# Performance work log

Measured on AMD Instinct MI355X. Metric: run time of the kernel, lower is better.

## Reference

```python
import jax, jax.numpy as jnp
import numpy as np

BATCH, NVIS, NHID, NCOND = 4096, 1024, 4096, 512


def setup_inputs() -> dict:
    key = jax.random.key(0)
    ks = jax.random.split(key, 6)
    return {
        "visible_data": jax.random.uniform(ks[0], (BATCH, NVIS), dtype=jnp.float32),
        "cond_data": jax.random.normal(ks[1], (BATCH, NCOND), dtype=jnp.float32),
        # uniform noise replaces torch.bernoulli's internal RNG: sample = (noise < p)
        "noise": jax.random.uniform(ks[2], (BATCH, NHID), dtype=jnp.float32),
        "W": jax.random.normal(ks[3], (NVIS, NHID), dtype=jnp.float32) * 0.1,
        "b": jnp.zeros((1, NVIS), dtype=jnp.float32),
        "c": jnp.zeros((1, NHID), dtype=jnp.float32),
        "A": jax.random.normal(ks[4], (NCOND, NVIS), dtype=jnp.float32) * 0.1,
        "B": jax.random.normal(ks[5], (NCOND, NHID), dtype=jnp.float32) * 0.1,
    }


def reference(visible_data, cond_data, noise, W, b, c, A, B):
    # sample_h_given_vu: sigmoid(v@W + u@B + c), bernoulli sample via uniform noise
    h1_mean = jax.nn.sigmoid(visible_data @ W + cond_data @ B + c)  # [B, nhid]
    h1_sample = (noise < h1_mean).astype(h1_mean.dtype)
    # sample_v_given_hu (binary): L1-normalized exp == softmax, then argmax one-hot
    pre = h1_sample @ W.T + cond_data @ A + b  # [B, nvis]
    v1_mean = jax.nn.softmax(pre, axis=1)
    max_idx = jnp.argmax(v1_mean, axis=1)
    v1_sample = jax.nn.one_hot(max_idx, pre.shape[1], dtype=pre.dtype)
    return v1_sample
```

## Files before the change

kernel.cpp:

```cpp
#include <hip/hip_runtime.h>
#include <math.h>

static constexpr int BATCH = 4096;
static constexpr int NVIS  = 1024;
static constexpr int NHID  = 4096;
static constexpr int NCOND = 512;

typedef __attribute__((ext_vector_type(8))) short bf16x8;
typedef __attribute__((ext_vector_type(4))) float f32x4;
typedef __attribute__((ext_vector_type(4))) int   i32x4;

static constexpr unsigned HCAP = 131072;
static constexpr unsigned RCAP = 256;
static constexpr size_t MB = 1u << 20;

static constexpr size_t F_WT0   = 0;
static constexpr size_t F_WT1   = F_WT0  + 8*MB;
static constexpr size_t F_BMT0  = F_WT1  + 8*MB;
static constexpr size_t F_BMT1  = F_BMT0 + 4*MB;
static constexpr size_t F_AT0   = F_BMT1 + 4*MB;
static constexpr size_t F_AT1   = F_AT0  + 1*MB;
static constexpr size_t F_V0    = F_AT1  + 1*MB;
static constexpr size_t F_V1    = F_V0   + 8*MB;
static constexpr size_t F_U0    = F_V1   + 8*MB;
static constexpr size_t F_U1    = F_U0   + 4*MB;
static constexpr size_t F_QH    = F_U1   + 4*MB;
static constexpr size_t F_QL    = F_QH   + 4*MB;
static constexpr size_t F_SINV  = F_QL   + 4*MB;
static constexpr size_t F_H     = F_SINV + 8*MB;
static constexpr size_t F_BB    = F_H    + 32*MB;
static constexpr size_t F_HFLAG = F_BB   + 1*MB;
static constexpr size_t F_RFLAG = F_HFLAG + 512*1024;
static constexpr size_t F_RBEST = F_RFLAG + 16384;
static constexpr size_t F_CNT   = F_RBEST + 16384;
static constexpr size_t F_PREB  = F_CNT  + 256;
static constexpr size_t WS_FULL = F_PREB + 2*MB;

__device__ __forceinline__ void gload16(const void* g, void* l) {
    __builtin_amdgcn_global_load_lds(
        (const __attribute__((address_space(1))) void*)g,
        (__attribute__((address_space(3))) void*)l, 16, 0, 0);
}

__device__ __forceinline__ void split1(float x, unsigned short& hi, unsigned short& lo) {
    unsigned u = __float_as_uint(x);
    unsigned r = u + 0x7FFFu + ((u >> 16) & 1u);
    hi = (unsigned short)(r >> 16);
    float rem = x - __uint_as_float(r & 0xFFFF0000u);
    unsigned u2 = __float_as_uint(rem);
    unsigned r2 = u2 + 0x7FFFu + ((u2 >> 16) & 1u);
    lo = (unsigned short)(r2 >> 16);
}

__device__ __forceinline__ void merge3(float& b, unsigned& ix, float& s,
                                       float b2, unsigned i2, float s2) {
    if (b2 > b || (b2 == b && i2 < ix)) { s = fmaxf(b, s2); b = b2; ix = i2; }
    else                                { s = fmaxf(s, b2); }
}

__global__ void kz_zero(unsigned* c) { if (threadIdx.x < 64) c[threadIdx.x] = 0; }

__global__ __launch_bounds__(256) void transpose_split(
    const float* __restrict__ src, int R, int C,
    unsigned short* __restrict__ d0, unsigned short* __restrict__ d1) {
    __shared__ float tile[32][33];
    const int c0 = blockIdx.x * 32, r0 = blockIdx.y * 32;
    const int tx = threadIdx.x & 31, ty = threadIdx.x >> 5;
#pragma unroll
    for (int e = 0; e < 4; ++e)
        tile[ty + e * 8][tx] = src[(size_t)(r0 + ty + e * 8) * C + c0 + tx];
    __syncthreads();
#pragma unroll
    for (int e = 0; e < 4; ++e) {
        int c = c0 + ty + e * 8;
        unsigned short hi, lo;
        split1(tile[tx][ty + e * 8], hi, lo);
        d0[(size_t)c * R + r0 + tx] = hi;
        d1[(size_t)c * R + r0 + tx] = lo;
    }
}

__global__ __launch_bounds__(256) void transpose_f32(
    const float* __restrict__ src, int R, int C, float* __restrict__ dst) {
    __shared__ float tile[32][33];
    const int c0 = blockIdx.x * 32, r0 = blockIdx.y * 32;
    const int tx = threadIdx.x & 31, ty = threadIdx.x >> 5;
#pragma unroll
    for (int e = 0; e < 4; ++e)
        tile[ty + e * 8][tx] = src[(size_t)(r0 + ty + e * 8) * C + c0 + tx];
    __syncthreads();
#pragma unroll
    for (int e = 0; e < 4; ++e)
        dst[(size_t)(c0 + ty + e * 8) * R + r0 + tx] = tile[tx][ty + e * 8];
}

__global__ __launch_bounds__(256) void split_planes(
    const float* __restrict__ src, int n4,
    unsigned short* __restrict__ p0, unsigned short* __restrict__ p1) {
    for (int i = blockIdx.x * 256 + threadIdx.x; i < n4; i += gridDim.x * 256) {
        float4 v = ((const float4*)src)[i];
        unsigned short h0,h1,h2,h3,l0,l1,l2,l3;
        split1(v.x,h0,l0); split1(v.y,h1,l1); split1(v.z,h2,l2); split1(v.w,h3,l3);
        ((ushort4*)p0)[i] = make_ushort4(h0,h1,h2,h3);
        ((ushort4*)p1)[i] = make_ushort4(l0,l1,l2,l3);
    }
}

__global__ __launch_bounds__(256) void quantize_w(
    const float* __restrict__ W, signed char* __restrict__ QH,
    signed char* __restrict__ QL, float* __restrict__ SINV) {
    __shared__ float red[256];
    const int i = blockIdx.x, t = threadIdx.x;
    const float* row = W + (size_t)i * NHID;
    float4 v[4];
    float mx = 0.f;
#pragma unroll
    for (int e = 0; e < 4; ++e) {
        v[e] = *(const float4*)(row + e * 1024 + t * 4);
        mx = fmaxf(mx, fmaxf(fmaxf(fabsf(v[e].x), fabsf(v[e].y)),
                             fmaxf(fabsf(v[e].z), fabsf(v[e].w))));
    }
    red[t] = mx; __syncthreads();
    for (int s = 128; s; s >>= 1) {
        if (t < s) red[t] = fmaxf(red[t], red[t + s]);
        __syncthreads();
    }
    const float rm = fmaxf(red[0], 1e-30f);
    const float sc = 32256.f / rm;
    if (t == 0) SINV[i] = rm / 32256.f;
#pragma unroll
    for (int e = 0; e < 4; ++e) {
        const float* pv = (const float*)&v[e];
        unsigned ph = 0, pl = 0;
#pragma unroll
        for (int j = 0; j < 4; ++j) {
            int wq = (int)lrintf(pv[j] * sc);
            int hi = (wq + 128) >> 8;
            int lo = wq - (hi << 8);
            ph |= ((unsigned)hi & 0xFFu) << (8 * j);
            pl |= ((unsigned)lo & 0xFFu) << (8 * j);
        }
        *(unsigned*)(QH + (size_t)i * NHID + e * 1024 + t * 4) = ph;
        *(unsigned*)(QL + (size_t)i * NHID + e * 1024 + t * 4) = pl;
    }
}

__global__ __launch_bounds__(512, 1) void k1_b64(
    const float* __restrict__ noise,
    const unsigned short* __restrict__ V0, const unsigned short* __restrict__ V1,
    const unsigned short* __restrict__ U0, const unsigned short* __restrict__ U1,
    const unsigned short* __restrict__ WT0, const unsigned short* __restrict__ WT1,
    const unsigned short* __restrict__ BmT0, const unsigned short* __restrict__ BmT1,
    const float* __restrict__ cvec, unsigned char* __restrict__ hout,
    unsigned* __restrict__ hcnt, unsigned* __restrict__ hflag)
{
    __shared__ __align__(16) unsigned short As0[256][64], As1[256][64],
                                            Bs0[256][64], Bs1[256][64];
    const int t = threadIdx.x, lane = t & 63, wid = t >> 6;
    const int g = lane >> 4, cc = lane & 15;
    const int wrow = wid >> 2, wcol = wid & 3;
    const int nwg = gridDim.x * gridDim.y;
    const int bid = blockIdx.y * gridDim.x + blockIdx.x;
    const int q = nwg >> 3;
    const int swz = (bid & 7) * q + (bid >> 3);
    const int b0 = (swz / gridDim.x) * 256;
    const int j0 = (swz % gridDim.x) * 256;

    f32x4 acc[8][4] = {};
    bf16x8 a0q[4], a1q[4];
    bf16x8 b0a[2][2], b1a[2][2];

    auto lba = [&](int r, int kk) {
        return (size_t)r * 128 + (size_t)(((kk << 2) | g) ^ (r & 7)) * 16;
    };
    auto readA = [&](int mh, int kk) {
#pragma unroll
        for (int k = 0; k < 4; ++k) {
            int r = wrow * 128 + (4 * mh + k) * 16 + cc;
            a0q[k] = *(const bf16x8*)((const char*)As0 + lba(r, kk));
            a1q[k] = *(const bf16x8*)((const char*)As1 + lba(r, kk));
        }
    };
    auto readB = [&](int nh, int kk) {
#pragma unroll
        for (int k = 0; k < 2; ++k) {
            int n = wcol * 64 + (2 * nh + k) * 16 + cc;
            b0a[nh][k] = *(const bf16x8*)((const char*)Bs0 + lba(n, kk));
            b1a[nh][k] = *(const bf16x8*)((const char*)Bs1 + lba(n, kk));
        }
    };
    auto mfma24 = [&](int mh, int nh) {
#pragma unroll
        for (int k = 0; k < 4; ++k)
#pragma unroll
            for (int n = 0; n < 2; ++n) {
                f32x4 c = acc[4 * mh + k][2 * nh + n];
                c = __builtin_amdgcn_mfma_f32_16x16x32_bf16(a0q[k], b0a[nh][n], c, 0, 0, 0);
                c = __builtin_amdgcn_mfma_f32_16x16x32_bf16(a0q[k], b1a[nh][n], c, 0, 0, 0);
                c = __builtin_amdgcn_mfma_f32_16x16x32_bf16(a1q[k], b0a[nh][n], c, 0, 0, 0);
                acc[4 * mh + k][2 * nh + n] = c;
            }
    };

    for (int tt = 0; tt < 24; ++tt) {
        const unsigned short *A0_, *A1_, *B0_, *B1_; int K_, k0_;
        if (tt < 16) { A0_ = V0; A1_ = V1; B0_ = WT0; B1_ = WT1; K_ = 1024; k0_ = tt * 64; }
        else         { A0_ = U0; A1_ = U1; B0_ = BmT0; B1_ = BmT1; K_ = 512; k0_ = (tt - 16) * 64; }
        __syncthreads();
#pragma unroll
        for (int e = 0; e < 4; ++e) {
            int idx = t + e * 512;
            int r = idx >> 3, p = idx & 7;
            int s = p ^ (r & 7);
            size_t ga = (size_t)(b0 + r) * K_ + k0_ + s * 8;
            size_t gb = (size_t)(j0 + r) * K_ + k0_ + s * 8;
            size_t ldd = (size_t)idx * 16;
            gload16(A0_ + ga, (char*)As0 + ldd);
            gload16(A1_ + ga, (char*)As1 + ldd);
            gload16(B0_ + gb, (char*)Bs0 + ldd);
            gload16(B1_ + gb, (char*)Bs1 + ldd);
        }
        __syncthreads();
#pragma unroll
        for (int kk = 0; kk < 2; ++kk) {
            readA(0, kk); readB(0, kk);
            __builtin_amdgcn_s_setprio(1); mfma24(0, 0); __builtin_amdgcn_s_setprio(0);
            readB(1, kk);
            __builtin_amdgcn_s_setprio(1); mfma24(0, 1); __builtin_amdgcn_s_setprio(0);
            readA(1, kk);
            __builtin_amdgcn_s_setprio(1); mfma24(1, 0); mfma24(1, 1); __builtin_amdgcn_s_setprio(0);
        }
    }

#pragma unroll
    for (int ni = 0; ni < 4; ++ni) {
        int j = j0 + wcol * 64 + ni * 16 + cc;
        float cj = cvec[j];
#pragma unroll
        for (int mi = 0; mi < 8; ++mi) {
#pragma unroll
            for (int i = 0; i < 4; ++i) {
                int b = b0 + wrow * 128 + mi * 16 + g * 4 + i;
                float z = acc[mi][ni][i] + cj;
                float m = 1.0f / (1.0f + __expf(-z));
                float nv = noise[(size_t)b * NHID + j];
                hout[(size_t)b * NHID + j] = (nv < m) ? (unsigned char)1 : (unsigned char)0;
                if (fabsf(nv - m) < 2.5e-4f) {
                    unsigned p = atomicAdd(hcnt, 1u);
                    if (p < HCAP) hflag[p] = ((unsigned)b << 12) | (unsigned)j;
                }
            }
        }
    }
}

__global__ __launch_bounds__(512, 2) void k2_i8(
    const unsigned char* __restrict__ hbf,
    const unsigned short* __restrict__ U0, const unsigned short* __restrict__ U1,
    const signed char* __restrict__ QH, const signed char* __restrict__ QL,
    const float* __restrict__ SINV,
    const unsigned short* __restrict__ AT0, const unsigned short* __restrict__ AT1,
    const float* __restrict__ bvec, float4* __restrict__ blockbest)
{
    __shared__ __align__(16) char smem[32768];
    __shared__ float4 mbuf[4][128];
    const int t = threadIdx.x, lane = t & 63, wid = t >> 6;
    const int g = lane >> 4, cc = lane & 15;
    const int wrow = wid >> 2, wcol = wid & 3;
    const int pcb = (g ^ ((cc >> 1) & 3)) * 16;
    const int nwg = gridDim.x * gridDim.y;
    const int bid = blockIdx.y * gridDim.x + blockIdx.x;
    const int q = nwg >> 3;
    const int swz = (bid & 7) * q + (bid >> 3);
    const int b0 = (swz / gridDim.x) * 128;
    const int i0 = (swz % gridDim.x) * 128;

    char* Ah  = smem;
    char* Qhs = smem + 8192;
    char* Qls = smem + 16384;

    i32x4 ah[4][2] = {}, al[4][2] = {};

    for (int k0 = 0; k0 < NHID; k0 += 64) {
        __syncthreads();
        {
            int r = t >> 2, s = t & 3, sc = s ^ ((r >> 1) & 3);
            size_t off = (size_t)r * 64 + s * 16;
            gload16(hbf + (size_t)(b0 + r) * NHID + k0 + sc * 16, Ah + off);
            gload16(QH + (size_t)(i0 + r) * NHID + k0 + sc * 16, Qhs + off);
            gload16(QL + (size_t)(i0 + r) * NHID + k0 + sc * 16, Qls + off);
        }
        __syncthreads();
        i32x4 bh[2], bl[2];
#pragma unroll
        for (int ni = 0; ni < 2; ++ni) {
            int n = wcol * 32 + ni * 16 + cc;
            bh[ni] = *(const i32x4*)(Qhs + (size_t)n * 64 + pcb);
            bl[ni] = *(const i32x4*)(Qls + (size_t)n * 64 + pcb);
        }
#pragma unroll
        for (int mi = 0; mi < 4; ++mi) {
            i32x4 a = *(const i32x4*)(Ah + (size_t)(wrow * 64 + mi * 16 + cc) * 64 + pcb);
#pragma unroll
            for (int ni = 0; ni < 2; ++ni) {
                ah[mi][ni] = __builtin_amdgcn_mfma_i32_16x16x64_i8(a, bh[ni], ah[mi][ni], 0, 0, 0);
                al[mi][ni] = __builtin_amdgcn_mfma_i32_16x16x64_i8(a, bl[ni], al[mi][ni], 0, 0, 0);
            }
        }
    }
    f32x4 acc[4][2];
#pragma unroll
    for (int ni = 0; ni < 2; ++ni) {
        int col = i0 + wcol * 32 + ni * 16 + cc;
        float sv = SINV[col];
#pragma unroll
        for (int mi = 0; mi < 4; ++mi)
#pragma unroll
            for (int e = 0; e < 4; ++e)
                acc[mi][ni][e] = fmaf(256.f, (float)ah[mi][ni][e], (float)al[mi][ni][e]) * sv;
    }

    char* As0 = smem;
    char* As1 = smem + 8192;
    char* Bs0 = smem + 16384;
    char* Bs1 = smem + 24576;
    for (int k0 = 0; k0 < NCOND; k0 += 32) {
        __syncthreads();
        {
            int r = t >> 2, s = t & 3, sc = s ^ ((r >> 1) & 3);
            size_t off = (size_t)r * 64 + s * 16;
            size_t ga = (size_t)(b0 + r) * NCOND + k0 + sc * 8;
            gload16(U0 + ga, As0 + off);
            gload16(U1 + ga, As1 + off);
            size_t go = (size_t)(i0 + r) * NCOND + k0 + sc * 8;
            gload16(AT0 + go, Bs0 + off);
            gload16(AT1 + go, Bs1 + off);
        }
        __syncthreads();
        bf16x8 bb0[2], bb1[2];
#pragma unroll
        for (int ni = 0; ni < 2; ++ni) {
            int n = wcol * 32 + ni * 16 + cc;
            bb0[ni] = *(const bf16x8*)(Bs0 + (size_t)n * 64 + pcb);
            bb1[ni] = *(const bf16x8*)(Bs1 + (size_t)n * 64 + pcb);
        }
#pragma unroll
        for (int mi = 0; mi < 4; ++mi) {
            int r = wrow * 64 + mi * 16 + cc;
            bf16x8 a0 = *(const bf16x8*)(As0 + (size_t)r * 64 + pcb);
            bf16x8 a1 = *(const bf16x8*)(As1 + (size_t)r * 64 + pcb);
#pragma unroll
            for (int ni = 0; ni < 2; ++ni) {
                acc[mi][ni] = __builtin_amdgcn_mfma_f32_16x16x32_bf16(a0, bb0[ni], acc[mi][ni], 0, 0, 0);
                acc[mi][ni] = __builtin_amdgcn_mfma_f32_16x16x32_bf16(a0, bb1[ni], acc[mi][ni], 0, 0, 0);
                acc[mi][ni] = __builtin_amdgcn_mfma_f32_16x16x32_bf16(a1, bb0[ni], acc[mi][ni], 0, 0, 0);
            }
        }
    }

#pragma unroll
    for (int ni = 0; ni < 2; ++ni) {
        int colb = i0 + wcol * 32 + ni * 16 + cc;
        float bb = bvec[colb];
#pragma unroll
        for (int mi = 0; mi < 4; ++mi)
#pragma unroll
            for (int i = 0; i < 4; ++i) acc[mi][ni][i] += bb;
    }
#pragma unroll
    for (int mi = 0; mi < 4; ++mi) {
#pragma unroll
        for (int i = 0; i < 4; ++i) {
            float best = acc[mi][0][i];
            unsigned bidx = (unsigned)(i0 + wcol * 32 + cc);
            float sec = -3.4e38f;
            merge3(best, bidx, sec, acc[mi][1][i],
                   (unsigned)(i0 + wcol * 32 + 16 + cc), -3.4e38f);
#pragma unroll
            for (int m = 1; m < 16; m <<= 1) {
                float ob = __shfl_xor(best, m);
                unsigned oi = __shfl_xor(bidx, m);
                float os = __shfl_xor(sec, m);
                merge3(best, bidx, sec, ob, oi, os);
            }
            if (cc == 0)
                mbuf[wcol][wrow * 64 + mi * 16 + g * 4 + i] =
                    make_float4(best, sec, __uint_as_float(bidx), 0.f);
        }
    }
    __syncthreads();
    if (t < 128) {
        float4 f0 = mbuf[0][t];
        float best = f0.x, sec = f0.y;
        unsigned bidx = __float_as_uint(f0.z);
#pragma unroll
        for (int wq = 1; wq < 4; ++wq) {
            float4 fq = mbuf[wq][t];
            merge3(best, bidx, sec, fq.x, __float_as_uint(fq.z), fq.y);
        }
        blockbest[(size_t)(b0 + t) * 8 + (unsigned)(i0 >> 7)] =
            make_float4(best, sec, __uint_as_float(bidx), 0.f);
    }
}

__global__ __launch_bounds__(256) void k5_recheck_h(
    const float* __restrict__ vd, const float* __restrict__ cd, const float* __restrict__ noise,
    const float* __restrict__ WTf, const float* __restrict__ BmTf, const float* __restrict__ cvec,
    const unsigned* __restrict__ hcnt, const unsigned* __restrict__ hflag,
    unsigned char* __restrict__ h) {
    const int gw = (blockIdx.x * 256 + threadIdx.x) >> 6, lane = threadIdx.x & 63;
    const int nw = gridDim.x * 4;
    unsigned n = *hcnt; if (n > HCAP) n = HCAP;
    for (unsigned e = gw; e < n; e += nw) {
        unsigned p = hflag[e];
        int b = p >> 12, j = p & 4095;
        double s = 0.0;
        for (int k = lane; k < NVIS; k += 64)
            s += (double)vd[(size_t)b * NVIS + k] * (double)WTf[(size_t)j * NVIS + k];
        for (int k = lane; k < NCOND; k += 64)
            s += (double)cd[(size_t)b * NCOND + k] * (double)BmTf[(size_t)j * NCOND + k];
        for (int m = 32; m; m >>= 1) s += __shfl_xor(s, m);
        if (lane == 0) {
            double z = s + (double)cvec[j];
            double mm = 1.0 / (1.0 + exp(-z));
            h[(size_t)b * NHID + j] =
                ((double)noise[(size_t)b * NHID + j] < mm) ? (unsigned char)1 : (unsigned char)0;
        }
    }
}

__global__ __launch_bounds__(256) void k3_merge8(
    const float4* __restrict__ blockbest, unsigned* __restrict__ rowbest,
    unsigned* __restrict__ rcnt, unsigned* __restrict__ rowflag) {
    const int t = threadIdx.x;
    const int row = blockIdx.x * 32 + (t >> 3), e = t & 7;
    float4 f = blockbest[(size_t)row * 8 + e];
    float best = f.x, sec = f.y;
    unsigned idx = __float_as_uint(f.z);
#pragma unroll
    for (int m = 1; m < 8; m <<= 1) {
        float ob = __shfl_xor(best, m);
        unsigned oi = __shfl_xor(idx, m);
        float os = __shfl_xor(sec, m);
        merge3(best, idx, sec, ob, oi, os);
    }
    if (e == 0) {
        rowbest[row] = idx;
        if (best - sec < 4e-3f) {
            unsigned p = atomicAdd(rcnt, 1u);
            if (p < 4096) rowflag[p] = (unsigned)row;
        }
    }
}

__global__ __launch_bounds__(256) void k_onehot(const unsigned* __restrict__ rowbest,
                                                float* __restrict__ out) {
    const int row = blockIdx.x;
    const unsigned idx = rowbest[row];
    const int base = threadIdx.x * 4;
    float4 o;
    o.x = (base + 0 == (int)idx) ? 1.f : 0.f;
    o.y = (base + 1 == (int)idx) ? 1.f : 0.f;
    o.z = (base + 2 == (int)idx) ? 1.f : 0.f;
    o.w = (base + 3 == (int)idx) ? 1.f : 0.f;
    *(float4*)(out + (size_t)row * NVIS + base) = o;
}

__global__ __launch_bounds__(256) void k6_rows_pre(
    const unsigned char* __restrict__ h, const float* __restrict__ cd,
    const float* __restrict__ W, const float* __restrict__ ATf, const float* __restrict__ bvec,
    const unsigned* __restrict__ rcnt, const unsigned* __restrict__ rowflag,
    double* __restrict__ prebuf) {
    const int gw = (blockIdx.x * 256 + threadIdx.x) >> 6, lane = threadIdx.x & 63;
    const int nw = gridDim.x * 4;
    unsigned n = *rcnt; if (n > RCAP) n = RCAP;
    for (unsigned e = gw; e < n * 1024u; e += nw) {
        int ri = e >> 10, i = e & 1023;
        int b = (int)rowflag[ri];
        double s = 0.0;
        for (int k = lane; k < NHID; k += 64) {
            double hv = h[(size_t)b * NHID + k] ? 1.0 : 0.0;
            s += hv * (double)W[(size_t)i * NHID + k];
        }
        for (int k = lane; k < NCOND; k += 64)
            s += (double)cd[(size_t)b * NCOND + k] * (double)ATf[(size_t)i * NCOND + k];
        for (int m = 32; m; m >>= 1) s += __shfl_xor(s, m);
        if (lane == 0) prebuf[(size_t)ri * 1024 + i] = s + (double)bvec[i];
    }
}

__global__ __launch_bounds__(256) void k6_rows_argmax(
    const unsigned* __restrict__ rcnt, const unsigned* __restrict__ rowflag,
    const double* __restrict__ prebuf, float* __restrict__ out) {
    __shared__ double sv[256];
    __shared__ int si[256];
    unsigned n = *rcnt; if (n > RCAP) n = RCAP;
    const int t = threadIdx.x;
    for (unsigned ri = blockIdx.x; ri < n; ri += gridDim.x) {
        const int row = (int)rowflag[ri];
        const double* pr = prebuf + (size_t)ri * 1024;
        double best = pr[t * 4];
        int bi = t * 4;
#pragma unroll
        for (int e = 1; e < 4; ++e) {
            double v = pr[t * 4 + e];
            if (v > best) { best = v; bi = t * 4 + e; }
        }
        sv[t] = best; si[t] = bi;
        __syncthreads();
        for (int s = 128; s; s >>= 1) {
            if (t < s) {
                double v2 = sv[t + s]; int i2 = si[t + s];
                if (v2 > sv[t] || (v2 == sv[t] && i2 < si[t])) { sv[t] = v2; si[t] = i2; }
            }
            __syncthreads();
        }
        const int amax = si[0];
        const int base = t * 4;
        float4 o;
        o.x = (base + 0 == amax) ? 1.f : 0.f;
        o.y = (base + 1 == amax) ? 1.f : 0.f;
        o.z = (base + 2 == amax) ? 1.f : 0.f;
        o.w = (base + 3 == amax) ? 1.f : 0.f;
        *(float4*)(out + (size_t)row * NVIS + base) = o;
        __syncthreads();
    }
}

extern "C" void kernel_launch(void* const* d_in, const int* in_sizes, int n_in,
                              void* d_out, int out_size, void* d_ws, size_t ws_size,
                              hipStream_t stream) {
    const float* vd = (const float*)d_in[0];
    const float* cd = (const float*)d_in[1];
    const float* nz = (const float*)d_in[2];
    const float* W  = (const float*)d_in[3];
    const float* bv = (const float*)d_in[4];
    const float* cv = (const float*)d_in[5];
    const float* Am = (const float*)d_in[6];
    const float* Bm = (const float*)d_in[7];
    float* out = (float*)d_out;
    char* w = (char*)d_ws;

    unsigned short* WT0  = (unsigned short*)(w + F_WT0);
    unsigned short* WT1  = (unsigned short*)(w + F_WT1);
    unsigned short* BmT0 = (unsigned short*)(w + F_BMT0);
    unsigned short* BmT1 = (unsigned short*)(w + F_BMT1);
    unsigned short* AT0  = (unsigned short*)(w + F_AT0);
    unsigned short* AT1  = (unsigned short*)(w + F_AT1);
    unsigned short* V0   = (unsigned short*)(w + F_V0);
    unsigned short* V1   = (unsigned short*)(w + F_V1);
    unsigned short* U0   = (unsigned short*)(w + F_U0);
    unsigned short* U1   = (unsigned short*)(w + F_U1);
    signed char*    QH   = (signed char*)(w + F_QH);
    signed char*    QL   = (signed char*)(w + F_QL);
    float*          SINV = (float*)(w + F_SINV);
    unsigned char*  hbf  = (unsigned char*)(w + F_H);
    float4*   blockbest  = (float4*)(w + F_BB);
    unsigned* hflag      = (unsigned*)(w + F_HFLAG);
    unsigned* rowflag    = (unsigned*)(w + F_RFLAG);
    unsigned* rowbest    = (unsigned*)(w + F_RBEST);
    unsigned* counters   = (unsigned*)(w + F_CNT);
    double*   prebuf     = (double*)(w + F_PREB);
    unsigned* hcnt = &counters[0];
    unsigned* rcnt = &counters[1];
    float* WTf32  = (float*)(w + F_V0);
    float* BmTf32 = (float*)(w + F_WT0);
    float* ATf32  = (float*)(w + F_WT1);

    dim3 blk(256);
    kz_zero<<<1, 64, 0, stream>>>(counters);
    transpose_split<<<dim3(NHID / 32, NVIS / 32), blk, 0, stream>>>(W, NVIS, NHID, WT0, WT1);
    transpose_split<<<dim3(NHID / 32, NCOND / 32), blk, 0, stream>>>(Bm, NCOND, NHID, BmT0, BmT1);
    transpose_split<<<dim3(NVIS / 32, NCOND / 32), blk, 0, stream>>>(Am, NCOND, NVIS, AT0, AT1);
    split_planes<<<2048, blk, 0, stream>>>(vd, BATCH * NVIS / 4, V0, V1);
    split_planes<<<2048, blk, 0, stream>>>(cd, BATCH * NCOND / 4, U0, U1);
    quantize_w<<<NVIS, blk, 0, stream>>>(W, QH, QL, SINV);
    k1_b64<<<dim3(NHID / 256, BATCH / 256), 512, 0, stream>>>(
        nz, V0, V1, U0, U1, WT0, WT1, BmT0, BmT1, cv, hbf, hcnt, hflag);
    transpose_f32<<<dim3(NHID / 32, NVIS / 32), blk, 0, stream>>>(W, NVIS, NHID, WTf32);
    transpose_f32<<<dim3(NHID / 32, NCOND / 32), blk, 0, stream>>>(Bm, NCOND, NHID, BmTf32);
    transpose_f32<<<dim3(NVIS / 32, NCOND / 32), blk, 0, stream>>>(Am, NCOND, NVIS, ATf32);
    k5_recheck_h<<<256, blk, 0, stream>>>(vd, cd, nz, WTf32, BmTf32, cv, hcnt, hflag, hbf);
    k2_i8<<<dim3(NVIS / 128, BATCH / 128), 512, 0, stream>>>(
        hbf, U0, U1, QH, QL, SINV, AT0, AT1, bv, blockbest);
    k3_merge8<<<BATCH / 32, blk, 0, stream>>>(blockbest, rowbest, rcnt, rowflag);
    k_onehot<<<BATCH, blk, 0, stream>>>(rowbest, out);
    k6_rows_pre<<<512, blk, 0, stream>>>(hbf, cd, W, ATf32, bv, rcnt, rowflag, prebuf);
    k6_rows_argmax<<<64, blk, 0, stream>>>(rcnt, rowflag, prebuf, out);
}
```

Baseline: 505.0 us.

## Fuse visible-data bf16 split into smaller-tile k1 GEMM, merge f32 transposes

The first GEMM kernel now reads fp32 visible and conditional data directly and splits each value into hi/lo bf16 planes while staging it to shared memory. This removes the separate split_planes pass and the V0/V1 workspace round-trip. The tile shrinks from 256x256 with 512 threads to 128x128 with 256 threads, a K step of 32 and up to four blocks per CU, trading operand reuse for occupancy. The three fp32 transposes are merged into one launch to cut launch overhead. The risk is the extra convert work inside the GEMM and lower arithmetic intensity per tile.

```diff
diff --git a/kernel.cpp b/kernel.cpp
--- a/kernel.cpp
+++ b/kernel.cpp
@@ -80,10 +80,16 @@
     }
 }
 
-__global__ __launch_bounds__(256) void transpose_f32(
-    const float* __restrict__ src, int R, int C, float* __restrict__ dst) {
+__global__ __launch_bounds__(256) void transpose_f32_all(
+    const float* __restrict__ W, const float* __restrict__ Bm, const float* __restrict__ Am,
+    float* __restrict__ WTf, float* __restrict__ BmTf, float* __restrict__ ATf) {
     __shared__ float tile[32][33];
-    const int c0 = blockIdx.x * 32, r0 = blockIdx.y * 32;
+    int blk = blockIdx.x;
+    const float* src; float* dst; int R, C, bx, by;
+    if (blk < 4096)      { src = W;  dst = WTf;  R = 1024; C = 4096; blk -= 0;    bx = blk & 127; by = blk >> 7; }
+    else if (blk < 6144) { src = Bm; dst = BmTf; R = 512;  C = 4096; blk -= 4096; bx = blk & 127; by = blk >> 7; }
+    else                 { src = Am; dst = ATf;  R = 512;  C = 1024; blk -= 6144; bx = blk & 31;  by = blk >> 5; }
+    const int c0 = bx * 32, r0 = by * 32;
     const int tx = threadIdx.x & 31, ty = threadIdx.x >> 5;
 #pragma unroll
     for (int e = 0; e < 4; ++e)
@@ -145,90 +151,76 @@
     }
 }
 
-__global__ __launch_bounds__(512, 1) void k1_b64(
+__global__ __launch_bounds__(256, 4) void k1_s4(
+    const float* __restrict__ vd, const float* __restrict__ cd,
     const float* __restrict__ noise,
-    const unsigned short* __restrict__ V0, const unsigned short* __restrict__ V1,
-    const unsigned short* __restrict__ U0, const unsigned short* __restrict__ U1,
     const unsigned short* __restrict__ WT0, const unsigned short* __restrict__ WT1,
     const unsigned short* __restrict__ BmT0, const unsigned short* __restrict__ BmT1,
     const float* __restrict__ cvec, unsigned char* __restrict__ hout,
     unsigned* __restrict__ hcnt, unsigned* __restrict__ hflag)
 {
-    __shared__ __align__(16) unsigned short As0[256][64], As1[256][64],
-                                            Bs0[256][64], Bs1[256][64];
+    __shared__ __align__(16) unsigned short As0[128][32], As1[128][32],
+                                            Bs0[128][32], Bs1[128][32];
     const int t = threadIdx.x, lane = t & 63, wid = t >> 6;
     const int g = lane >> 4, cc = lane & 15;
-    const int wrow = wid >> 2, wcol = wid & 3;
+    const int wrow = wid >> 1, wcol = wid & 1;
+    const int pc = (g ^ ((cc >> 1) & 3)) * 8;
     const int nwg = gridDim.x * gridDim.y;
     const int bid = blockIdx.y * gridDim.x + blockIdx.x;
     const int q = nwg >> 3;
     const int swz = (bid & 7) * q + (bid >> 3);
-    const int b0 = (swz / gridDim.x) * 256;
-    const int j0 = (swz % gridDim.x) * 256;
-
-    f32x4 acc[8][4] = {};
-    bf16x8 a0q[4], a1q[4];
-    bf16x8 b0a[2][2], b1a[2][2];
-
-    auto lba = [&](int r, int kk) {
-        return (size_t)r * 128 + (size_t)(((kk << 2) | g) ^ (r & 7)) * 16;
-    };
-    auto readA = [&](int mh, int kk) {
-#pragma unroll
-        for (int k = 0; k < 4; ++k) {
-            int r = wrow * 128 + (4 * mh + k) * 16 + cc;
-            a0q[k] = *(const bf16x8*)((const char*)As0 + lba(r, kk));
-            a1q[k] = *(const bf16x8*)((const char*)As1 + lba(r, kk));
-        }
-    };
-    auto readB = [&](int nh, int kk) {
-#pragma unroll
-        for (int k = 0; k < 2; ++k) {
-            int n = wcol * 64 + (2 * nh + k) * 16 + cc;
-            b0a[nh][k] = *(const bf16x8*)((const char*)Bs0 + lba(n, kk));
-            b1a[nh][k] = *(const bf16x8*)((const char*)Bs1 + lba(n, kk));
-        }
-    };
-    auto mfma24 = [&](int mh, int nh) {
-#pragma unroll
-        for (int k = 0; k < 4; ++k)
-#pragma unroll
-            for (int n = 0; n < 2; ++n) {
-                f32x4 c = acc[4 * mh + k][2 * nh + n];
-                c = __builtin_amdgcn_mfma_f32_16x16x32_bf16(a0q[k], b0a[nh][n], c, 0, 0, 0);
-                c = __builtin_amdgcn_mfma_f32_16x16x32_bf16(a0q[k], b1a[nh][n], c, 0, 0, 0);
-                c = __builtin_amdgcn_mfma_f32_16x16x32_bf16(a1q[k], b0a[nh][n], c, 0, 0, 0);
-                acc[4 * mh + k][2 * nh + n] = c;
-            }
-    };
-
-    for (int tt = 0; tt < 24; ++tt) {
-        const unsigned short *A0_, *A1_, *B0_, *B1_; int K_, k0_;
-        if (tt < 16) { A0_ = V0; A1_ = V1; B0_ = WT0; B1_ = WT1; K_ = 1024; k0_ = tt * 64; }
-        else         { A0_ = U0; A1_ = U1; B0_ = BmT0; B1_ = BmT1; K_ = 512; k0_ = (tt - 16) * 64; }
-        __syncthreads();
-#pragma unroll
-        for (int e = 0; e < 4; ++e) {
-            int idx = t + e * 512;
-            int r = idx >> 3, p = idx & 7;
-            int s = p ^ (r & 7);
-            size_t ga = (size_t)(b0 + r) * K_ + k0_ + s * 8;
-            size_t gb = (size_t)(j0 + r) * K_ + k0_ + s * 8;
-            size_t ldd = (size_t)idx * 16;
-            gload16(A0_ + ga, (char*)As0 + ldd);
-            gload16(A1_ + ga, (char*)As1 + ldd);
-            gload16(B0_ + gb, (char*)Bs0 + ldd);
-            gload16(B1_ + gb, (char*)Bs1 + ldd);
-        }
-        __syncthreads();
-#pragma unroll
-        for (int kk = 0; kk < 2; ++kk) {
-            readA(0, kk); readB(0, kk);
-            __builtin_amdgcn_s_setprio(1); mfma24(0, 0); __builtin_amdgcn_s_setprio(0);
-            readB(1, kk);
-            __builtin_amdgcn_s_setprio(1); mfma24(0, 1); __builtin_amdgcn_s_setprio(0);
-            readA(1, kk);
-            __builtin_amdgcn_s_setprio(1); mfma24(1, 0); mfma24(1, 1); __builtin_amdgcn_s_setprio(0);
+    const int b0 = (swz / gridDim.x) * 128;
+    const int j0 = (swz % gridDim.x) * 128;
+
+    f32x4 acc[4][4] = {};
+
+    for (int ph = 0; ph < 2; ++ph) {
+        const int K = ph ? NCOND : NVIS;
+        const float* Asrc = ph ? cd : vd;
+        const unsigned short* B0 = ph ? BmT0 : WT0;
+        const unsigned short* B1 = ph ? BmT1 : WT1;
+        for (int k0 = 0; k0 < K; k0 += 32) {
+            __syncthreads();
+#pragma unroll
+            for (int e = 0; e < 4; ++e) {
+                int idx = t + e * 256, row = idx >> 3, qq = idx & 7;
+                const float4 v = *(const float4*)(Asrc + (size_t)(b0 + row) * K + k0 + qq * 4);
+                unsigned short h0,h1,h2,h3, s0,s1,s2,s3;
+                split1(v.x,h0,s0); split1(v.y,h1,s1); split1(v.z,h2,s2); split1(v.w,h3,s3);
+                int c = qq >> 1, sc = c ^ ((row >> 1) & 3);
+                int pos = sc * 8 + (qq & 1) * 4;
+                *(ushort4*)&As0[row][pos] = make_ushort4(h0,h1,h2,h3);
+                *(ushort4*)&As1[row][pos] = make_ushort4(s0,s1,s2,s3);
+            }
+#pragma unroll
+            for (int e = 0; e < 2; ++e) {
+                int idx = t + e * 256, r = idx >> 2, s = idx & 3;
+                int sc = s ^ ((r >> 1) & 3);
+                size_t gb = (size_t)(j0 + r) * K + k0 + sc * 8;
+                size_t ldd = (size_t)idx * 8;
+                gload16(B0 + gb, &Bs0[0][0] + ldd);
+                gload16(B1 + gb, &Bs1[0][0] + ldd);
+            }
+            __syncthreads();
+            bf16x8 bb0[4], bb1[4];
+#pragma unroll
+            for (int ni = 0; ni < 4; ++ni) {
+                int n = wcol * 64 + ni * 16 + cc;
+                bb0[ni] = *(const bf16x8*)&Bs0[n][pc];
+                bb1[ni] = *(const bf16x8*)&Bs1[n][pc];
+            }
+#pragma unroll
+            for (int mi = 0; mi < 4; ++mi) {
+                int r = wrow * 64 + mi * 16 + cc;
+                bf16x8 a0 = *(const bf16x8*)&As0[r][pc];
+                bf16x8 a1 = *(const bf16x8*)&As1[r][pc];
+#pragma unroll
+                for (int ni = 0; ni < 4; ++ni) {
+                    acc[mi][ni] = __builtin_amdgcn_mfma_f32_16x16x32_bf16(a0, bb0[ni], acc[mi][ni], 0, 0, 0);
+                    acc[mi][ni] = __builtin_amdgcn_mfma_f32_16x16x32_bf16(a0, bb1[ni], acc[mi][ni], 0, 0, 0);
+                    acc[mi][ni] = __builtin_amdgcn_mfma_f32_16x16x32_bf16(a1, bb0[ni], acc[mi][ni], 0, 0, 0);
+                }
+            }
         }
     }
 
@@ -237,10 +229,10 @@
         int j = j0 + wcol * 64 + ni * 16 + cc;
         float cj = cvec[j];
 #pragma unroll
-        for (int mi = 0; mi < 8; ++mi) {
+        for (int mi = 0; mi < 4; ++mi) {
 #pragma unroll
             for (int i = 0; i < 4; ++i) {
-                int b = b0 + wrow * 128 + mi * 16 + g * 4 + i;
+                int b = b0 + wrow * 64 + mi * 16 + g * 4 + i;
                 float z = acc[mi][ni][i] + cj;
                 float m = 1.0f / (1.0f + __expf(-z));
                 float nv = noise[(size_t)b * NHID + j];
@@ -547,8 +539,6 @@
     unsigned short* BmT1 = (unsigned short*)(w + F_BMT1);
     unsigned short* AT0  = (unsigned short*)(w + F_AT0);
     unsigned short* AT1  = (unsigned short*)(w + F_AT1);
-    unsigned short* V0   = (unsigned short*)(w + F_V0);
-    unsigned short* V1   = (unsigned short*)(w + F_V1);
     unsigned short* U0   = (unsigned short*)(w + F_U0);
     unsigned short* U1   = (unsigned short*)(w + F_U1);
     signed char*    QH   = (signed char*)(w + F_QH);
@@ -572,14 +562,11 @@
     transpose_split<<<dim3(NHID / 32, NVIS / 32), blk, 0, stream>>>(W, NVIS, NHID, WT0, WT1);
     transpose_split<<<dim3(NHID / 32, NCOND / 32), blk, 0, stream>>>(Bm, NCOND, NHID, BmT0, BmT1);
     transpose_split<<<dim3(NVIS / 32, NCOND / 32), blk, 0, stream>>>(Am, NCOND, NVIS, AT0, AT1);
-    split_planes<<<2048, blk, 0, stream>>>(vd, BATCH * NVIS / 4, V0, V1);
     split_planes<<<2048, blk, 0, stream>>>(cd, BATCH * NCOND / 4, U0, U1);
     quantize_w<<<NVIS, blk, 0, stream>>>(W, QH, QL, SINV);
-    k1_b64<<<dim3(NHID / 256, BATCH / 256), 512, 0, stream>>>(
-        nz, V0, V1, U0, U1, WT0, WT1, BmT0, BmT1, cv, hbf, hcnt, hflag);
-    transpose_f32<<<dim3(NHID / 32, NVIS / 32), blk, 0, stream>>>(W, NVIS, NHID, WTf32);
-    transpose_f32<<<dim3(NHID / 32, NCOND / 32), blk, 0, stream>>>(Bm, NCOND, NHID, BmTf32);
-    transpose_f32<<<dim3(NVIS / 32, NCOND / 32), blk, 0, stream>>>(Am, NCOND, NVIS, ATf32);
+    k1_s4<<<dim3(NHID / 128, BATCH / 128), blk, 0, stream>>>(
+        vd, cd, nz, WT0, WT1, BmT0, BmT1, cv, hbf, hcnt, hflag);
+    transpose_f32_all<<<6656, blk, 0, stream>>>(W, Bm, Am, WTf32, BmTf32, ATf32);
     k5_recheck_h<<<256, blk, 0, stream>>>(vd, cd, nz, WTf32, BmTf32, cv, hcnt, hflag, hbf);
     k2_i8<<<dim3(NVIS / 128, BATCH / 128), 512, 0, stream>>>(
         hbf, U0, U1, QH, QL, SINV, AT0, AT1, bv, blockbest);
```

Result: slower. 574.3 us (+13.7%).
